# Performance work log

Measured on AMD Instinct MI355X. Metric: run time of the kernel, lower is better.

## Reference

```python
import jax, jax.numpy as jnp
import numpy as np

L, N, D = 2, 100000, 128
TRACE_HID, MVC_DIM, MVC_HID = 256, 128, 64
NUM_EDGE = 1600000
TAU = 0.5


def setup_inputs() -> dict:
    key = jax.random.key(0)
    ks = jax.random.split(key, 9)
    trace_all = jax.random.normal(ks[0], (L, N, D), dtype=jnp.float32)
    W_lin = jax.random.normal(ks[1], (TRACE_HID, L * D), dtype=jnp.float32) * 0.05
    W_lin2 = jax.random.normal(ks[2], (MVC_DIM, TRACE_HID), dtype=jnp.float32) * 0.05
    W_fc1 = jax.random.normal(ks[3], (MVC_HID, 2 * MVC_DIM), dtype=jnp.float32) * 0.05
    b_fc1 = jax.random.normal(ks[4], (MVC_HID,), dtype=jnp.float32) * 0.05
    W_fc2 = jax.random.normal(ks[5], (2, MVC_HID), dtype=jnp.float32) * 0.05
    b_fc2 = jax.random.normal(ks[6], (2,), dtype=jnp.float32) * 0.05
    u = jax.random.uniform(ks[7], (NUM_EDGE, 2), dtype=jnp.float32, minval=1e-6, maxval=1.0 - 1e-6)
    gumbel = -jnp.log(-jnp.log(u))  # standard Gumbel(0,1) noise
    edge_index = jax.random.randint(ks[8], (2, 3 * NUM_EDGE), 0, N, dtype=jnp.int32)
    return {
        "trace_all": trace_all, "W_lin": W_lin, "W_lin2": W_lin2,
        "W_fc1": W_fc1, "b_fc1": b_fc1, "W_fc2": W_fc2, "b_fc2": b_fc2,
        "gumbel": gumbel, "edge_index": edge_index, "num_edge": NUM_EDGE,
    }


def reference(trace_all, W_lin, W_lin2, W_fc1, b_fc1, W_fc2, b_fc2, gumbel, edge_index, num_edge):
    # --- TraceMLP: [L, N, d] -> mvc [N, mvc_dim] (eval mode: dropout is identity)
    l, n, d = trace_all.shape
    x = jnp.transpose(trace_all, (1, 0, 2)).reshape(n, l * d)      # [N, L*d]
    h = jax.nn.relu(x @ W_lin.T)                                   # [N, trace_hidden]
    mvc = h @ W_lin2.T                                             # [N, mvc_dim]
    norm = jnp.maximum(jnp.linalg.norm(mvc, axis=1, keepdims=True), 1e-12)
    mvc = mvc / norm                                               # F.normalize(p=2, dim=1)

    # --- EdgeScoringNet over non-slow edges (first num_edge columns)
    src = edge_index[0, :num_edge]
    dst = edge_index[1, :num_edge]
    comb = jnp.concatenate([mvc[src], mvc[dst]], axis=1)           # [E, 2*mvc_dim]
    h2 = jax.nn.relu(comb @ W_fc1.T + b_fc1)                       # [E, mvc_hidden]
    scores = h2 @ W_fc2.T + b_fc2                                  # [E, 2]

    # --- gumbel_softmax(tau=0.5, hard=True)[:, 0] (straight-through)
    y_soft = jax.nn.softmax((scores + gumbel) / TAU, axis=-1)
    y_hard = jax.nn.one_hot(jnp.argmax(y_soft, axis=-1), 2, dtype=y_soft.dtype)
    ret = y_hard - jax.lax.stop_gradient(y_soft) + y_soft
    active = ret[:, 0]                                             # [E], values in {0,1}

    # --- train_mask: first block = active, next two blocks = 1 - active
    train_mask = jnp.concatenate([active, 1.0 - active, 1.0 - active])  # [3*E]
    return train_mask
```

## Files before the change

kernel.cpp:

```cpp
#include <hip/hip_runtime.h>

#define NN   100000
#define EE   1600000
#define EROW 4800000

typedef _Float16 half8 __attribute__((ext_vector_type(8)));
typedef _Float16 half4 __attribute__((ext_vector_type(4)));
typedef float    f32x4 __attribute__((ext_vector_type(4)));

__device__ __forceinline__ float4 ld4(const float* p){ return *(const float4*)p; }

__device__ __forceinline__ unsigned splitf(float v) {
    _Float16 h = (_Float16)v;
    float r = v - (float)h;
    _Float16 l = (_Float16)(r * 2048.0f);
    union { _Float16 f; unsigned short u; } uh, ul;
    uh.f = h; ul.f = l;
    return (unsigned)uh.u | ((unsigned)ul.u << 16);
}

__global__ __launch_bounds__(256)
void prep_w(const float* __restrict__ W1, const float* __restrict__ W2,
            const float* __restrict__ W3, unsigned* __restrict__ o1,
            unsigned* __restrict__ o2, unsigned* __restrict__ o3)
{
    int idx = blockIdx.x * 256 + threadIdx.x;
    if (idx < 65536) {
        o1[idx] = splitf(W1[idx]);
    } else if (idx < 98304) {
        int i = idx - 65536;
        o2[i] = splitf(W2[i]);
    } else {
        int i = idx - 98304;
        int j = i >> 7, k = i & 127;
        o3[i] = splitf(W3[(j & 63) * 256 + (j >> 6) * 128 + k]);
    }
}

template<int SRCA, int EPI>
__global__ __launch_bounds__(256, 2)
void gemm_mfma(const void* __restrict__ Asrc, const unsigned* __restrict__ Bw,
               const float* __restrict__ bias, unsigned* __restrict__ outS,
               float* __restrict__ outF, unsigned short* __restrict__ outH,
               int M, int K, int No)
{
    __shared__ __align__(16) _Float16 Ah[2][128][40];
    __shared__ __align__(16) _Float16 Al[2][128][40];
    __shared__ __align__(16) _Float16 Bh[2][128][40];
    __shared__ __align__(16) _Float16 Bl[2][128][40];
    float* sqv = (float*)&Ah[0][0][0];

    const int t     = threadIdx.x;
    const int wm    = (t >> 6) >> 1;
    const int wn    = (t >> 6) & 1;
    const int lane  = t & 63;
    const int lm    = lane & 15;
    const int q     = lane >> 4;
    const int mBase = blockIdx.x * 128;
    const int nBase = blockIdx.y * 128;

    const int srow = t >> 3;
    const int sseg = (t & 7) * 4;

    f32x4 aH[4][4], aM[4][4];
#pragma unroll
    for (int i = 0; i < 4; ++i)
#pragma unroll
        for (int j = 0; j < 4; ++j) {
            aH[i][j] = (f32x4){0.f, 0.f, 0.f, 0.f};
            aM[i][j] = (f32x4){0.f, 0.f, 0.f, 0.f};
        }

    uint2 sAh[4], sAl[4], sBh[4], sBl[4];

    auto loadStage = [&](int k0) {
#pragma unroll
        for (int it = 0; it < 4; ++it) {
            const int row = srow + it * 32;
            int rg = mBase + row; rg = rg < M ? rg : M - 1;
            if (SRCA == 0) {
                const int k = k0 + sseg;
                const float* ap = (const float*)Asrc
                    + (size_t)(k >> 7) * ((size_t)NN * 128)
                    + (size_t)rg * 128 + (k & 127);
                float4 f = ld4(ap);
                unsigned p0 = splitf(f.x), p1 = splitf(f.y);
                unsigned p2 = splitf(f.z), p3 = splitf(f.w);
                sAh[it].x = (p0 & 0xffffu) | (p1 << 16);
                sAh[it].y = (p2 & 0xffffu) | (p3 << 16);
                sAl[it].x = (p0 >> 16) | (p1 & 0xffff0000u);
                sAl[it].y = (p2 >> 16) | (p3 & 0xffff0000u);
            } else {
                const unsigned* ap = (const unsigned*)Asrc + (size_t)rg * K + k0 + sseg;
                uint4 u = *(const uint4*)ap;
                sAh[it].x = (u.x & 0xffffu) | (u.y << 16);
                sAh[it].y = (u.z & 0xffffu) | (u.w << 16);
                sAl[it].x = (u.x >> 16) | (u.y & 0xffff0000u);
                sAl[it].y = (u.z >> 16) | (u.w & 0xffff0000u);
            }
            const unsigned* bp = Bw + (size_t)(nBase + row) * K + k0 + sseg;
            uint4 ub = *(const uint4*)bp;
            sBh[it].x = (ub.x & 0xffffu) | (ub.y << 16);
            sBh[it].y = (ub.z & 0xffffu) | (ub.w << 16);
            sBl[it].x = (ub.x >> 16) | (ub.y & 0xffff0000u);
            sBl[it].y = (ub.z >> 16) | (ub.w & 0xffff0000u);
        }
    };

    loadStage(0);
    const int nk = K / 32;
    for (int kt = 0; kt < nk; ++kt) {
        const int b = kt & 1;
#pragma unroll
        for (int it = 0; it < 4; ++it) {
            const int row = srow + it * 32;
            *(uint2*)&Ah[b][row][sseg] = sAh[it];
            *(uint2*)&Al[b][row][sseg] = sAl[it];
            *(uint2*)&Bh[b][row][sseg] = sBh[it];
            *(uint2*)&Bl[b][row][sseg] = sBl[it];
        }
        __syncthreads();
        if (kt + 1 < nk) loadStage((kt + 1) * 32);

        half8 fAh[4], fAl[4], fBh[4], fBl[4];
#pragma unroll
        for (int i = 0; i < 4; ++i) {
            fAh[i] = *(const half8*)&Ah[b][wm * 64 + i * 16 + lm][q * 8];
            fAl[i] = *(const half8*)&Al[b][wm * 64 + i * 16 + lm][q * 8];
            fBh[i] = *(const half8*)&Bh[b][wn * 64 + i * 16 + lm][q * 8];
            fBl[i] = *(const half8*)&Bl[b][wn * 64 + i * 16 + lm][q * 8];
        }
#pragma unroll
        for (int i = 0; i < 4; ++i)
#pragma unroll
            for (int j = 0; j < 4; ++j)
                aH[i][j] = __builtin_amdgcn_mfma_f32_16x16x32_f16(fAh[i], fBh[j], aH[i][j], 0, 0, 0);
#pragma unroll
        for (int i = 0; i < 4; ++i)
#pragma unroll
            for (int j = 0; j < 4; ++j)
                aM[i][j] = __builtin_amdgcn_mfma_f32_16x16x32_f16(fAh[i], fBl[j], aM[i][j], 0, 0, 0);
#pragma unroll
        for (int i = 0; i < 4; ++i)
#pragma unroll
            for (int j = 0; j < 4; ++j)
                aM[i][j] = __builtin_amdgcn_mfma_f32_16x16x32_f16(fAl[i], fBh[j], aM[i][j], 0, 0, 0);
    }

    const float cM = 1.0f / 2048.0f;
#pragma unroll
    for (int i = 0; i < 4; ++i)
#pragma unroll
        for (int j = 0; j < 4; ++j)
            aH[i][j] = aH[i][j] + aM[i][j] * cM;

    float nm[4][4];
    if (EPI == 1) {
        __syncthreads();
#pragma unroll
        for (int i = 0; i < 4; ++i)
#pragma unroll
            for (int r = 0; r < 4; ++r) {
                float s = 0.f;
#pragma unroll
                for (int j = 0; j < 4; ++j) { float x = aH[i][j][r]; s = fmaf(x, x, s); }
#pragma unroll
                for (int off = 1; off < 16; off <<= 1) s += __shfl_xor(s, off, 16);
                if (lm == 0) sqv[(wm * 64 + i * 16 + q * 4 + r) * 2 + wn] = s;
            }
        __syncthreads();
#pragma unroll
        for (int i = 0; i < 4; ++i)
#pragma unroll
            for (int r = 0; r < 4; ++r) {
                const int rl = wm * 64 + i * 16 + q * 4 + r;
                nm[i][r] = fmaxf(sqrtf(sqv[rl * 2] + sqv[rl * 2 + 1]), 1e-12f);
            }
    }

    float bj[4] = {0.f, 0.f, 0.f, 0.f};
    if (EPI == 2 && wn == 0) {
#pragma unroll
        for (int j = 0; j < 4; ++j) bj[j] = bias[j * 16 + lm];
    }

#pragma unroll
    for (int i = 0; i < 4; ++i)
#pragma unroll
        for (int r = 0; r < 4; ++r) {
            const int m = mBase + wm * 64 + i * 16 + q * 4 + r;
            if (m < M) {
#pragma unroll
                for (int j = 0; j < 4; ++j) {
                    const int c = nBase + wn * 64 + j * 16 + lm;
                    float v = aH[i][j][r];
                    if (EPI == 0) { v = fmaxf(v, 0.f); outS[(size_t)m * No + c] = splitf(v); }
                    if (EPI == 1) { v = v / nm[i][r];  outS[(size_t)m * No + c] = splitf(v); }
                    if (EPI == 2) {
                        v += bj[j];
                        outF[(size_t)m * No + c] = v;
                        union { _Float16 f; unsigned short u; } cv; cv.f = (_Float16)v;
                        outH[(size_t)m * No + c] = cv.u;
                    }
                }
            }
        }
}

#define EPB 128
__global__ __launch_bounds__(256, 4)
void edge_k(const unsigned short* __restrict__ pH, const float* __restrict__ p,
            const int* __restrict__ ei, const float* __restrict__ gum,
            const float* __restrict__ W2, const float* __restrict__ b2,
            float* __restrict__ out)
{
    __shared__ int   sidx[EPB];
    __shared__ int   didx[EPB];
    __shared__ float gl[2 * EPB];
    __shared__ float act[EPB];

    const int t  = threadIdx.x;
    const int e0 = blockIdx.x * EPB;

    if (t < EPB) sidx[t] = ei[e0 + t];
    else         didx[t - EPB] = ei[EROW + e0 + (t - EPB)];
    gl[t] = gum[(size_t)e0 * 2 + t];
    __syncthreads();

    const int j   = t & 15;
    const int grp = t >> 4;
    const float4 w0 = ld4(&W2[j * 4]);
    const float4 w1 = ld4(&W2[64 + j * 4]);
    const float4 dk = make_float4(w0.x - w1.x, w0.y - w1.y,
                                  w0.z - w1.z, w0.w - w1.w);
    const float4 dw = make_float4(fabsf(dk.x), fabsf(dk.y),
                                  fabsf(dk.z), fabsf(dk.w));
    const float b20 = b2[0], b21 = b2[1];
    const float dB  = b20 - b21;

    union U8 { uint2 u; half4 h; };
    U8 ua[8], ub[8];
#pragma unroll
    for (int it = 0; it < 8; ++it) {
        const int el = grp * 8 + it;
        ua[it].u = *(const uint2*)&pH[(size_t)sidx[el] * 128 + j * 4];
        ub[it].u = *(const uint2*)&pH[(size_t)didx[el] * 128 + 64 + j * 4];
    }

#pragma unroll
    for (int it = 0; it < 8; ++it) {
        const int el = grp * 8 + it;
        const float a0 = (float)ua[it].h[0], a1 = (float)ua[it].h[1];
        const float a2 = (float)ua[it].h[2], a3 = (float)ua[it].h[3];
        const float c0 = (float)ub[it].h[0], c1 = (float)ub[it].h[1];
        const float c2 = (float)ub[it].h[2], c3 = (float)ub[it].h[3];
        const float r0 = fmaxf(a0 + c0, 0.f);
        const float r1 = fmaxf(a1 + c1, 0.f);
        const float r2 = fmaxf(a2 + c2, 0.f);
        const float r3 = fmaxf(a3 + c3, 0.f);
        float sc = r0 * dk.x + r1 * dk.y + r2 * dk.z + r3 * dk.w;
        float eb = dw.x * (fabsf(a0) + fabsf(c0)) + dw.y * (fabsf(a1) + fabsf(c1))
                 + dw.z * (fabsf(a2) + fabsf(c2)) + dw.w * (fabsf(a3) + fabsf(c3));
#pragma unroll
        for (int off = 1; off < 16; off <<= 1) {
            sc += __shfl_xor(sc, off, 16);
            eb += __shfl_xor(eb, off, 16);
        }
        const float g0 = gl[el * 2], g1 = gl[el * 2 + 1];
        const float gap = sc + dB + (g0 - g1);
        const float bound = eb * 0.0009765625f + 2e-5f;
        float av;
        if (fabsf(gap) > bound) {
            av = (gap >= 0.f) ? 1.f : 0.f;
        } else {
            const float4 pa = ld4(&p[(size_t)sidx[el] * 128 + j * 4]);
            const float4 pb = ld4(&p[(size_t)didx[el] * 128 + 64 + j * 4]);
            const float q0 = fmaxf(pa.x + pb.x, 0.f);
            const float q1 = fmaxf(pa.y + pb.y, 0.f);
            const float q2 = fmaxf(pa.z + pb.z, 0.f);
            const float q3 = fmaxf(pa.w + pb.w, 0.f);
            float t0 = q0 * w0.x + q1 * w0.y + q2 * w0.z + q3 * w0.w;
            float t1 = q0 * w1.x + q1 * w1.y + q2 * w1.z + q3 * w1.w;
#pragma unroll
            for (int off = 1; off < 16; off <<= 1) {
                t0 += __shfl_xor(t0, off, 16);
                t1 += __shfl_xor(t1, off, 16);
            }
            const float ge = (t0 + b20 + g0) - (t1 + b21 + g1);
            av = (ge >= 0.f) ? 1.f : 0.f;
        }
        if (j == 0) act[el] = av;
    }
    __syncthreads();

    if (t < EPB) {
        const float a = act[t];
        const size_t e = (size_t)e0 + t;
        out[e]                  = a;
        out[EE + e]             = 1.f - a;
        out[2 * (size_t)EE + e] = 1.f - a;
    }
}

extern "C" void kernel_launch(void* const* d_in, const int* in_sizes, int n_in,
                              void* d_out, int out_size, void* d_ws, size_t ws_size,
                              hipStream_t stream)
{
    const float* trace  = (const float*)d_in[0];
    const float* W_lin  = (const float*)d_in[1];
    const float* W_lin2 = (const float*)d_in[2];
    const float* W_fc1  = (const float*)d_in[3];
    const float* b_fc1  = (const float*)d_in[4];
    const float* W_fc2  = (const float*)d_in[5];
    const float* b_fc2  = (const float*)d_in[6];
    const float* gum    = (const float*)d_in[7];
    const int*   ei     = (const int*)  d_in[8];
    float*       out    = (float*)d_out;

    char* ws = (char*)d_ws;
    unsigned*       hpl = (unsigned*)ws;
    unsigned*       mpl = (unsigned*)(ws + (size_t)NN * 256 * 4);
    unsigned*       W1i = (unsigned*)(ws + (size_t)NN * 256 * 4 + (size_t)NN * 128 * 4);
    unsigned*       W2i = W1i + 65536;
    unsigned*       W3i = W2i + 32768;
    float*          p   = (float*)ws;
    unsigned short* pH  = (unsigned short*)(ws + (size_t)NN * 128 * 4);

    prep_w<<<448, 256, 0, stream>>>(W_lin, W_lin2, W_fc1, W1i, W2i, W3i);

    const int mB = (NN + 127) / 128;

    gemm_mfma<0, 0><<<dim3(mB, 2), 256, 0, stream>>>(trace, W1i, nullptr, hpl, nullptr, nullptr, NN, 256, 256);
    gemm_mfma<1, 1><<<dim3(mB, 1), 256, 0, stream>>>(hpl, W2i, nullptr, mpl, nullptr, nullptr, NN, 256, 128);
    gemm_mfma<1, 2><<<dim3(mB, 1), 256, 0, stream>>>(mpl, W3i, b_fc1, nullptr, p, pH, NN, 128, 128);
    edge_k<<<EE / EPB, 256, 0, stream>>>(pH, p, ei, gum, W_fc2, b_fc2, out);
}
```

Baseline: 373.0 us.

## Prefetch A two stages ahead, stream B fragments, and raise MFMA priority

```diff
diff --git a/kernel.cpp b/kernel.cpp
--- a/kernel.cpp
+++ b/kernel.cpp
@@ -71,9 +71,9 @@
             aM[i][j] = (f32x4){0.f, 0.f, 0.f, 0.f};
         }
 
-    uint2 sAh[4], sAl[4], sBh[4], sBl[4];
-
-    auto loadStage = [&](int k0) {
+    uint2 sAh[2][4], sAl[2][4], sBh[4], sBl[4];
+
+    auto loadA = [&](int set, int k0) {
 #pragma unroll
         for (int it = 0; it < 4; ++it) {
             const int row = srow + it * 32;
@@ -86,18 +86,25 @@
                 float4 f = ld4(ap);
                 unsigned p0 = splitf(f.x), p1 = splitf(f.y);
                 unsigned p2 = splitf(f.z), p3 = splitf(f.w);
-                sAh[it].x = (p0 & 0xffffu) | (p1 << 16);
-                sAh[it].y = (p2 & 0xffffu) | (p3 << 16);
-                sAl[it].x = (p0 >> 16) | (p1 & 0xffff0000u);
-                sAl[it].y = (p2 >> 16) | (p3 & 0xffff0000u);
+                sAh[set][it].x = (p0 & 0xffffu) | (p1 << 16);
+                sAh[set][it].y = (p2 & 0xffffu) | (p3 << 16);
+                sAl[set][it].x = (p0 >> 16) | (p1 & 0xffff0000u);
+                sAl[set][it].y = (p2 >> 16) | (p3 & 0xffff0000u);
             } else {
                 const unsigned* ap = (const unsigned*)Asrc + (size_t)rg * K + k0 + sseg;
                 uint4 u = *(const uint4*)ap;
-                sAh[it].x = (u.x & 0xffffu) | (u.y << 16);
-                sAh[it].y = (u.z & 0xffffu) | (u.w << 16);
-                sAl[it].x = (u.x >> 16) | (u.y & 0xffff0000u);
-                sAl[it].y = (u.z >> 16) | (u.w & 0xffff0000u);
-            }
+                sAh[set][it].x = (u.x & 0xffffu) | (u.y << 16);
+                sAh[set][it].y = (u.z & 0xffffu) | (u.w << 16);
+                sAl[set][it].x = (u.x >> 16) | (u.y & 0xffff0000u);
+                sAl[set][it].y = (u.z >> 16) | (u.w & 0xffff0000u);
+            }
+        }
+    };
+
+    auto loadB = [&](int k0) {
+#pragma unroll
+        for (int it = 0; it < 4; ++it) {
+            const int row = srow + it * 32;
             const unsigned* bp = Bw + (size_t)(nBase + row) * K + k0 + sseg;
             uint4 ub = *(const uint4*)bp;
             sBh[it].x = (ub.x & 0xffffu) | (ub.y << 16);
@@ -107,44 +114,45 @@
         }
     };
 
-    loadStage(0);
     const int nk = K / 32;
+    loadA(0, 0);
+    loadB(0);
+    if (nk > 1) loadA(1, 32);
+
     for (int kt = 0; kt < nk; ++kt) {
         const int b = kt & 1;
+        const int s = kt & 1;
 #pragma unroll
         for (int it = 0; it < 4; ++it) {
             const int row = srow + it * 32;
-            *(uint2*)&Ah[b][row][sseg] = sAh[it];
-            *(uint2*)&Al[b][row][sseg] = sAl[it];
+            *(uint2*)&Ah[b][row][sseg] = sAh[s][it];
+            *(uint2*)&Al[b][row][sseg] = sAl[s][it];
             *(uint2*)&Bh[b][row][sseg] = sBh[it];
             *(uint2*)&Bl[b][row][sseg] = sBl[it];
         }
         __syncthreads();
-        if (kt + 1 < nk) loadStage((kt + 1) * 32);
-
-        half8 fAh[4], fAl[4], fBh[4], fBl[4];
+        if (kt + 1 < nk) loadB((kt + 1) * 32);
+        if (kt + 2 < nk) loadA(s, (kt + 2) * 32);
+
+        half8 fAh[4], fAl[4];
 #pragma unroll
         for (int i = 0; i < 4; ++i) {
             fAh[i] = *(const half8*)&Ah[b][wm * 64 + i * 16 + lm][q * 8];
             fAl[i] = *(const half8*)&Al[b][wm * 64 + i * 16 + lm][q * 8];
-            fBh[i] = *(const half8*)&Bh[b][wn * 64 + i * 16 + lm][q * 8];
-            fBl[i] = *(const half8*)&Bl[b][wn * 64 + i * 16 + lm][q * 8];
-        }
-#pragma unroll
-        for (int i = 0; i < 4; ++i)
-#pragma unroll
-            for (int j = 0; j < 4; ++j)
-                aH[i][j] = __builtin_amdgcn_mfma_f32_16x16x32_f16(fAh[i], fBh[j], aH[i][j], 0, 0, 0);
-#pragma unroll
-        for (int i = 0; i < 4; ++i)
-#pragma unroll
-            for (int j = 0; j < 4; ++j)
-                aM[i][j] = __builtin_amdgcn_mfma_f32_16x16x32_f16(fAh[i], fBl[j], aM[i][j], 0, 0, 0);
-#pragma unroll
-        for (int i = 0; i < 4; ++i)
-#pragma unroll
-            for (int j = 0; j < 4; ++j)
-                aM[i][j] = __builtin_amdgcn_mfma_f32_16x16x32_f16(fAl[i], fBh[j], aM[i][j], 0, 0, 0);
+        }
+        __builtin_amdgcn_s_setprio(1);
+#pragma unroll
+        for (int j = 0; j < 4; ++j) {
+            half8 fBh = *(const half8*)&Bh[b][wn * 64 + j * 16 + lm][q * 8];
+            half8 fBl = *(const half8*)&Bl[b][wn * 64 + j * 16 + lm][q * 8];
+#pragma unroll
+            for (int i = 0; i < 4; ++i) {
+                aH[i][j] = __builtin_amdgcn_mfma_f32_16x16x32_f16(fAh[i], fBh, aH[i][j], 0, 0, 0);
+                aM[i][j] = __builtin_amdgcn_mfma_f32_16x16x32_f16(fAh[i], fBl, aM[i][j], 0, 0, 0);
+                aM[i][j] = __builtin_amdgcn_mfma_f32_16x16x32_f16(fAl[i], fBh, aM[i][j], 0, 0, 0);
+            }
+        }
+        __builtin_amdgcn_s_setprio(0);
     }
 
     const float cM = 1.0f / 2048.0f;
```

New measurement: 447.0 us. +19.9%, slower.

## Load MFMA fragments directly from global memory, dropping LDS staging

Applied to the files above, without the earlier changes.

```diff
diff --git a/kernel.cpp b/kernel.cpp
--- a/kernel.cpp
+++ b/kernel.cpp
@@ -37,18 +37,14 @@
     }
 }
 
-template<int SRCA, int EPI>
+template<int SRCA, int EPI, int K>
 __global__ __launch_bounds__(256, 2)
 void gemm_mfma(const void* __restrict__ Asrc, const unsigned* __restrict__ Bw,
                const float* __restrict__ bias, unsigned* __restrict__ outS,
                float* __restrict__ outF, unsigned short* __restrict__ outH,
-               int M, int K, int No)
+               int M, int No)
 {
-    __shared__ __align__(16) _Float16 Ah[2][128][40];
-    __shared__ __align__(16) _Float16 Al[2][128][40];
-    __shared__ __align__(16) _Float16 Bh[2][128][40];
-    __shared__ __align__(16) _Float16 Bl[2][128][40];
-    float* sqv = (float*)&Ah[0][0][0];
+    __shared__ float sqv[128][2];
 
     const int t     = threadIdx.x;
     const int wm    = (t >> 6) >> 1;
@@ -59,9 +55,6 @@
     const int mBase = blockIdx.x * 128;
     const int nBase = blockIdx.y * 128;
 
-    const int srow = t >> 3;
-    const int sseg = (t & 7) * 4;
-
     f32x4 aH[4][4], aM[4][4];
 #pragma unroll
     for (int i = 0; i < 4; ++i)
@@ -71,65 +64,79 @@
             aM[i][j] = (f32x4){0.f, 0.f, 0.f, 0.f};
         }
 
-    uint2 sAh[4], sAl[4], sBh[4], sBl[4];
-
-    auto loadStage = [&](int k0) {
-#pragma unroll
-        for (int it = 0; it < 4; ++it) {
-            const int row = srow + it * 32;
-            int rg = mBase + row; rg = rg < M ? rg : M - 1;
+    int arow[4], brow[4];
+#pragma unroll
+    for (int i = 0; i < 4; ++i) {
+        int r = mBase + wm * 64 + i * 16 + lm;
+        arow[i] = r < M ? r : M - 1;
+        brow[i] = nBase + wn * 64 + i * 16 + lm;
+    }
+
+    union HL { uint4 u; half8 h; };
+
+#pragma unroll
+    for (int kt = 0; kt < K / 32; ++kt) {
+        const int k0 = kt * 32 + q * 8;
+
+        half8 fAh[4], fAl[4], fBh[4], fBl[4];
+
+#pragma unroll
+        for (int i = 0; i < 4; ++i) {
+            HL H, L;
             if (SRCA == 0) {
-                const int k = k0 + sseg;
                 const float* ap = (const float*)Asrc
-                    + (size_t)(k >> 7) * ((size_t)NN * 128)
-                    + (size_t)rg * 128 + (k & 127);
-                float4 f = ld4(ap);
-                unsigned p0 = splitf(f.x), p1 = splitf(f.y);
-                unsigned p2 = splitf(f.z), p3 = splitf(f.w);
-                sAh[it].x = (p0 & 0xffffu) | (p1 << 16);
-                sAh[it].y = (p2 & 0xffffu) | (p3 << 16);
-                sAl[it].x = (p0 >> 16) | (p1 & 0xffff0000u);
-                sAl[it].y = (p2 >> 16) | (p3 & 0xffff0000u);
+                    + (size_t)(k0 >> 7) * ((size_t)NN * 128)
+                    + (size_t)arow[i] * 128 + (k0 & 127);
+                float4 f0 = ld4(ap);
+                float4 f1 = ld4(ap + 4);
+                unsigned p0 = splitf(f0.x), p1 = splitf(f0.y);
+                unsigned p2 = splitf(f0.z), p3 = splitf(f0.w);
+                unsigned p4 = splitf(f1.x), p5 = splitf(f1.y);
+                unsigned p6 = splitf(f1.z), p7 = splitf(f1.w);
+                H.u.x = (p0 & 0xffffu) | (p1 << 16);
+                H.u.y = (p2 & 0xffffu) | (p3 << 16);
+                H.u.z = (p4 & 0xffffu) | (p5 << 16);
+                H.u.w = (p6 & 0xffffu) | (p7 << 16);
+                L.u.x = (p0 >> 16) | (p1 & 0xffff0000u);
+                L.u.y = (p2 >> 16) | (p3 & 0xffff0000u);
+                L.u.z = (p4 >> 16) | (p5 & 0xffff0000u);
+                L.u.w = (p6 >> 16) | (p7 & 0xffff0000u);
             } else {
-                const unsigned* ap = (const unsigned*)Asrc + (size_t)rg * K + k0 + sseg;
-                uint4 u = *(const uint4*)ap;
-                sAh[it].x = (u.x & 0xffffu) | (u.y << 16);
-                sAh[it].y = (u.z & 0xffffu) | (u.w << 16);
-                sAl[it].x = (u.x >> 16) | (u.y & 0xffff0000u);
-                sAl[it].y = (u.z >> 16) | (u.w & 0xffff0000u);
-            }
-            const unsigned* bp = Bw + (size_t)(nBase + row) * K + k0 + sseg;
-            uint4 ub = *(const uint4*)bp;
-            sBh[it].x = (ub.x & 0xffffu) | (ub.y << 16);
-            sBh[it].y = (ub.z & 0xffffu) | (ub.w << 16);
-            sBl[it].x = (ub.x >> 16) | (ub.y & 0xffff0000u);
-            sBl[it].y = (ub.z >> 16) | (ub.w & 0xffff0000u);
-        }
-    };
-
-    loadStage(0);
-    const int nk = K / 32;
-    for (int kt = 0; kt < nk; ++kt) {
-        const int b = kt & 1;
-#pragma unroll
-        for (int it = 0; it < 4; ++it) {
-            const int row = srow + it * 32;
-            *(uint2*)&Ah[b][row][sseg] = sAh[it];
-            *(uint2*)&Al[b][row][sseg] = sAl[it];
-            *(uint2*)&Bh[b][row][sseg] = sBh[it];
-            *(uint2*)&Bl[b][row][sseg] = sBl[it];
-        }
-        __syncthreads();
-        if (kt + 1 < nk) loadStage((kt + 1) * 32);
-
-        half8 fAh[4], fAl[4], fBh[4], fBl[4];
-#pragma unroll
-        for (int i = 0; i < 4; ++i) {
-            fAh[i] = *(const half8*)&Ah[b][wm * 64 + i * 16 + lm][q * 8];
-            fAl[i] = *(const half8*)&Al[b][wm * 64 + i * 16 + lm][q * 8];
-            fBh[i] = *(const half8*)&Bh[b][wn * 64 + i * 16 + lm][q * 8];
-            fBl[i] = *(const half8*)&Bl[b][wn * 64 + i * 16 + lm][q * 8];
-        }
+                const unsigned* ap = (const unsigned*)Asrc + (size_t)arow[i] * K + k0;
+                uint4 u0 = *(const uint4*)ap;
+                uint4 u1 = *(const uint4*)(ap + 4);
+                H.u.x = (u0.x & 0xffffu) | (u0.y << 16);
+                H.u.y = (u0.z & 0xffffu) | (u0.w << 16);
+                H.u.z = (u1.x & 0xffffu) | (u1.y << 16);
+                H.u.w = (u1.z & 0xffffu) | (u1.w << 16);
+                L.u.x = (u0.x >> 16) | (u0.y & 0xffff0000u);
+                L.u.y = (u0.z >> 16) | (u0.w & 0xffff0000u);
+                L.u.z = (u1.x >> 16) | (u1.y & 0xffff0000u);
+                L.u.w = (u1.z >> 16) | (u1.w & 0xffff0000u);
+            }
+            fAh[i] = H.h;
+            fAl[i] = L.h;
+        }
+
+#pragma unroll
+        for (int j = 0; j < 4; ++j) {
+            const unsigned* bp = Bw + (size_t)brow[j] * K + k0;
+            uint4 u0 = *(const uint4*)bp;
+            uint4 u1 = *(const uint4*)(bp + 4);
+            HL H, L;
+            H.u.x = (u0.x & 0xffffu) | (u0.y << 16);
+            H.u.y = (u0.z & 0xffffu) | (u0.w << 16);
+            H.u.z = (u1.x & 0xffffu) | (u1.y << 16);
+            H.u.w = (u1.z & 0xffffu) | (u1.w << 16);
+            L.u.x = (u0.x >> 16) | (u0.y & 0xffff0000u);
+            L.u.y = (u0.z >> 16) | (u0.w & 0xffff0000u);
+            L.u.z = (u1.x >> 16) | (u1.y & 0xffff0000u);
+            L.u.w = (u1.z >> 16) | (u1.w & 0xffff0000u);
+            fBh[j] = H.h;
+            fBl[j] = L.h;
+        }
+
+        __builtin_amdgcn_s_setprio(1);
 #pragma unroll
         for (int i = 0; i < 4; ++i)
 #pragma unroll
@@ -145,6 +152,7 @@
 #pragma unroll
             for (int j = 0; j < 4; ++j)
                 aM[i][j] = __builtin_amdgcn_mfma_f32_16x16x32_f16(fAl[i], fBh[j], aM[i][j], 0, 0, 0);
+        __builtin_amdgcn_s_setprio(0);
     }
 
     const float cM = 1.0f / 2048.0f;
@@ -156,7 +164,6 @@
 
     float nm[4][4];
     if (EPI == 1) {
-        __syncthreads();
 #pragma unroll
         for (int i = 0; i < 4; ++i)
 #pragma unroll
@@ -166,7 +173,7 @@
                 for (int j = 0; j < 4; ++j) { float x = aH[i][j][r]; s = fmaf(x, x, s); }
 #pragma unroll
                 for (int off = 1; off < 16; off <<= 1) s += __shfl_xor(s, off, 16);
-                if (lm == 0) sqv[(wm * 64 + i * 16 + q * 4 + r) * 2 + wn] = s;
+                if (lm == 0) sqv[wm * 64 + i * 16 + q * 4 + r][wn] = s;
             }
         __syncthreads();
 #pragma unroll
@@ -174,7 +181,7 @@
 #pragma unroll
             for (int r = 0; r < 4; ++r) {
                 const int rl = wm * 64 + i * 16 + q * 4 + r;
-                nm[i][r] = fmaxf(sqrtf(sqv[rl * 2] + sqv[rl * 2 + 1]), 1e-12f);
+                nm[i][r] = fmaxf(sqrtf(sqv[rl][0] + sqv[rl][1]), 1e-12f);
             }
     }
 
@@ -330,8 +337,8 @@
 
     const int mB = (NN + 127) / 128;
 
-    gemm_mfma<0, 0><<<dim3(mB, 2), 256, 0, stream>>>(trace, W1i, nullptr, hpl, nullptr, nullptr, NN, 256, 256);
-    gemm_mfma<1, 1><<<dim3(mB, 1), 256, 0, stream>>>(hpl, W2i, nullptr, mpl, nullptr, nullptr, NN, 256, 128);
-    gemm_mfma<1, 2><<<dim3(mB, 1), 256, 0, stream>>>(mpl, W3i, b_fc1, nullptr, p, pH, NN, 128, 128);
+    gemm_mfma<0, 0, 256><<<dim3(mB, 2), 256, 0, stream>>>(trace, W1i, nullptr, hpl, nullptr, nullptr, NN, 256);
+    gemm_mfma<1, 1, 256><<<dim3(mB, 1), 256, 0, stream>>>(hpl, W2i, nullptr, mpl, nullptr, nullptr, NN, 128);
+    gemm_mfma<1, 2, 128><<<dim3(mB, 1), 256, 0, stream>>>(mpl, W3i, b_fc1, nullptr, p, pH, NN, 128);
     edge_k<<<EE / EPB, 256, 0, stream>>>(pH, p, ei, gum, W_fc2, b_fc2, out);
 }
```

Measured after the change: 434.7 us. +16.6%, slower.
